# Performance work log

Measured on AMD Instinct MI355X. Metric: run time of the kernel, lower is better.

## Reference

```python
import jax, jax.numpy as jnp
import numpy as np

B, S, DIM = 2, 2048, 1024
H, DH = 16, 64
WIN = 512


def setup_inputs() -> dict:
    key = jax.random.key(0)
    k1, k2, k3 = jax.random.split(key, 3)
    x = jax.random.normal(k1, (B, S, DIM), dtype=jnp.float32)
    Wqkv = jax.random.normal(k2, (DIM, 3 * H * DH), dtype=jnp.float32) * (DIM ** -0.5)
    Wout = jax.random.normal(k3, (H * DH, DIM), dtype=jnp.float32) * ((H * DH) ** -0.5)
    return {"x": x, "Wqkv": Wqkv, "Wout": Wout}


def reference(x, Wqkv, Wout):
    b, s, _ = x.shape
    qkv = jnp.einsum('bsd,de->bse', x, Wqkv)  # (B,S,3*H*DH)
    q, k, v = jnp.split(qkv, 3, axis=-1)
    # -> (B,H,S,DH)
    q = q.reshape(b, s, H, DH).transpose(0, 2, 1, 3)
    k = k.reshape(b, s, H, DH).transpose(0, 2, 1, 3)
    v = v.reshape(b, s, H, DH).transpose(0, 2, 1, 3)
    scale = DH ** -0.5  # attention sees per-head dim
    scores = jnp.einsum('bhsd,bhtd->bhst', q, k) * scale  # dense (B,H,S,S)
    i = jnp.arange(s)[:, None]
    j = jnp.arange(s)[None, :]
    mask = (j >= i - WIN + 1) & (j <= i)  # causal sliding window
    mask_value = -jnp.finfo(scores.dtype).max
    scores = jnp.where(mask[None, None], scores, mask_value)
    attn = jax.nn.softmax(scores, axis=-1)
    out = jnp.einsum('bhst,bhtd->bhsd', attn, v)
    out = out.transpose(0, 2, 1, 3).reshape(b, s, H * DH)
    return jnp.einsum('bse,ed->bsd', out, Wout)
```

## Files before the change

kernel.cpp:

```cpp
#include <hip/hip_runtime.h>

#define S_LEN 2048
#define BATCH 2
#define HDIM 1024
#define NH 16
#define DH 64
#define WINSZ 512
#define MROWS (BATCH * S_LEN)

typedef __attribute__((ext_vector_type(8))) short bfrag;
typedef __attribute__((ext_vector_type(4))) float f32x4;
typedef __attribute__((ext_vector_type(4))) int i128;

__device__ __forceinline__ short f2bf(float f) {
    union { float f; unsigned u; } v;
    v.f = f;
    unsigned r = v.u + 0x7fffu + ((v.u >> 16) & 1u);
    return (short)(r >> 16);
}

__device__ __forceinline__ void gload_lds16(const short* g, short* l) {
    __builtin_amdgcn_global_load_lds(
        (const __attribute__((address_space(1))) unsigned int*)g,
        (__attribute__((address_space(3))) unsigned int*)l, 16, 0, 0);
}

__global__ __launch_bounds__(256)
void prep_kernel(const float* __restrict__ x, const float* __restrict__ Wqkv,
                 const float* __restrict__ Wout,
                 short* __restrict__ x_bf, short* __restrict__ wqkv_t, short* __restrict__ wout_t)
{
    __shared__ float tile[32][33];
    const int bid = blockIdx.x;
    const int t = threadIdx.x;

    if (bid < 4096) {
        int i = bid * 256 + t;
        float4 v = ((const float4*)x)[i];
        union { short s[4]; int2 p; } u;
        u.s[0] = f2bf(v.x); u.s[1] = f2bf(v.y); u.s[2] = f2bf(v.z); u.s[3] = f2bf(v.w);
        ((int2*)x_bf)[i] = u.p;
        return;
    }

    const float* in;
    short* out;
    int R, C, bx, by;
    if (bid < 7168) {
        int lb = bid - 4096;
        in = Wqkv; out = wqkv_t; R = 1024; C = 3072;
        bx = lb % 96; by = lb / 96;
    } else {
        int lb = bid - 7168;
        in = Wout; out = wout_t; R = 1024; C = 1024;
        bx = lb & 31; by = lb >> 5;
    }
    int tc0 = bx * 32, tr0 = by * 32;
    int c = t & 31, r0 = t >> 5;
    #pragma unroll
    for (int k = 0; k < 4; ++k) {
        int r = r0 + k * 8;
        tile[r][c] = in[(size_t)(tr0 + r) * C + tc0 + c];
    }
    __syncthreads();
    int r2p = (t & 15) << 1, c0 = t >> 4;
    #pragma unroll
    for (int k = 0; k < 2; ++k) {
        int c2 = c0 + k * 16;
        union { short sh[2]; int w; } u;
        u.sh[0] = f2bf(tile[r2p][c2]);
        u.sh[1] = f2bf(tile[r2p + 1][c2]);
        *(int*)(&out[(size_t)(tc0 + c2) * R + tr0 + r2p]) = u.w;
    }
}

__global__ __launch_bounds__(256, 3)
void gemm_qkv(const short* __restrict__ A, const short* __restrict__ Bt,
              short* __restrict__ qk_rm, short* __restrict__ vto)
{
    __shared__ __align__(16) short smraw[17408];
    short (*Al)[4096] = (short(*)[4096])smraw;
    short (*Bl)[4096] = (short(*)[4096])(smraw + 8192);
    const int K = HDIM;
    const int t = threadIdx.x;
    const int lane = t & 63;
    const int wave = t >> 6;
    const int wr = wave >> 1, wc = wave & 1;
    const int m0 = blockIdx.y * 128, n0 = blockIdx.x * 128;
    const int lq = lane & 15;
    const int g = lane >> 4;
    const int lk8 = g << 3;

    f32x4 acc[4][4];
    #pragma unroll
    for (int m = 0; m < 4; ++m)
        #pragma unroll
        for (int n = 0; n < 4; ++n)
            acc[m][n] = (f32x4){0.f, 0.f, 0.f, 0.f};

    const int row0s = t >> 2, col0s = (t & 3) << 3;
    const int row1s = (256 + t) >> 2;
    const size_t dst0 = (size_t)(wave * 64) * 8;
    const size_t dst1 = (size_t)(256 + wave * 64) * 8;

    auto stage = [&](int k0, int sb) {
        gload_lds16(&A[(size_t)(m0 + row0s) * K + k0 + col0s], &Al[sb][0] + dst0);
        gload_lds16(&Bt[(size_t)(n0 + row0s) * K + k0 + col0s], &Bl[sb][0] + dst0);
        gload_lds16(&A[(size_t)(m0 + row1s) * K + k0 + col0s], &Al[sb][0] + dst1);
        gload_lds16(&Bt[(size_t)(n0 + row1s) * K + k0 + col0s], &Bl[sb][0] + dst1);
    };

    const int nk = K >> 5;
    stage(0, 0);
    __syncthreads();
    for (int ki = 0; ki < nk; ++ki) {
        const int cur = ki & 1;
        if (ki + 1 < nk) stage((ki + 1) << 5, cur ^ 1);
        bfrag af[4], bfr[4];
        #pragma unroll
        for (int m = 0; m < 4; ++m)
            af[m] = *(const bfrag*)(&Al[cur][(wr * 64 + m * 16 + lq) * 32 + lk8]);
        #pragma unroll
        for (int n = 0; n < 4; ++n)
            bfr[n] = *(const bfrag*)(&Bl[cur][(wc * 64 + n * 16 + lq) * 32 + lk8]);
        #pragma unroll
        for (int m = 0; m < 4; ++m)
            #pragma unroll
            for (int n = 0; n < 4; ++n)
                acc[m][n] = __builtin_amdgcn_mfma_f32_16x16x32_bf16(af[m], bfr[n], acc[m][n], 0, 0, 0);
        __syncthreads();
    }

    if (n0 < 2048) {
        #pragma unroll
        for (int m = 0; m < 4; ++m)
            #pragma unroll
            for (int n = 0; n < 4; ++n) {
                int col = n0 + wc * 64 + n * 16 + lq;
                int row0 = m0 + wr * 64 + m * 16 + g * 4;
                #pragma unroll
                for (int r = 0; r < 4; ++r)
                    qk_rm[(size_t)(row0 + r) * 2048 + col] = f2bf(acc[m][n][r]);
            }
    } else {
        short* T = smraw;
        #pragma unroll
        for (int m = 0; m < 4; ++m)
            #pragma unroll
            for (int n = 0; n < 4; ++n) {
                int cl = wc * 64 + n * 16 + lq;
                int rl0 = wr * 64 + m * 16 + g * 4;
                union { short sh[4]; int2 w; } u;
                #pragma unroll
                for (int r = 0; r < 4; ++r) u.sh[r] = f2bf(acc[m][n][r]);
                *(int2*)(&T[cl * 136 + rl0]) = u.w;
            }
        __syncthreads();
        const int b = m0 >> 11, sbase = m0 & 2047;
        const int h0 = (n0 - 2048) >> 6;
        #pragma unroll
        for (int i = 0; i < 8; ++i) {
            int c2 = i * 256 + t;
            int rv = c2 >> 4;
            int sc = (c2 & 15) << 3;
            int h = h0 + (rv >> 6), dh = rv & 63;
            i128 v = *(const i128*)(&T[rv * 136 + sc]);
            *(i128*)(&vto[((size_t)((b * NH + h) * DH + dh)) * S_LEN + sbase + sc]) = v;
        }
    }
}

__global__ __launch_bounds__(256, 2)
void gemm_out(const short* __restrict__ A, const short* __restrict__ Bt,
              float* __restrict__ co)
{
    __shared__ __align__(16) short Al[2][128 * 64];
    __shared__ __align__(16) short Bl[2][128 * 64];
    const int K = HDIM, N = HDIM;
    const int t = threadIdx.x;
    const int lane = t & 63;
    const int wave = t >> 6;
    const int wr = wave >> 1, wc = wave & 1;
    const int m0 = blockIdx.y * 128, n0 = blockIdx.x * 128;
    const int lq = lane & 15;
    const int g = lane >> 4;

    f32x4 acc[4][4];
    #pragma unroll
    for (int m = 0; m < 4; ++m)
        #pragma unroll
        for (int n = 0; n < 4; ++n)
            acc[m][n] = (f32x4){0.f, 0.f, 0.f, 0.f};

    auto stage = [&](int k0, int sb) {
        #pragma unroll
        for (int q = 0; q < 4; ++q) {
            int chunk = q * 256 + t;
            int row = chunk >> 3, col = (chunk & 7) << 3;
            size_t dst = (size_t)(q * 256 + wave * 64) * 8;
            gload_lds16(&A[(size_t)(m0 + row) * K + k0 + col], &Al[sb][0] + dst);
            gload_lds16(&Bt[(size_t)(n0 + row) * K + k0 + col], &Bl[sb][0] + dst);
        }
    };

    const int nk = K >> 6;
    stage(0, 0);
    for (int ki = 0; ki < nk; ++ki) {
        const int cur = ki & 1;
        if (ki + 1 < nk) {
            stage((ki + 1) << 6, cur ^ 1);
            asm volatile("s_waitcnt vmcnt(8)" ::: "memory");
        } else {
            asm volatile("s_waitcnt vmcnt(0)" ::: "memory");
        }
        __builtin_amdgcn_sched_barrier(0);
        __builtin_amdgcn_s_barrier();
        __builtin_amdgcn_sched_barrier(0);
        bfrag af[4][2], bfr[4][2];
        #pragma unroll
        for (int m = 0; m < 4; ++m)
            #pragma unroll
            for (int ks = 0; ks < 2; ++ks)
                af[m][ks] = *(const bfrag*)(&Al[cur][(wr * 64 + m * 16 + lq) * 64 + ks * 32 + (g << 3)]);
        #pragma unroll
        for (int n = 0; n < 4; ++n)
            #pragma unroll
            for (int ks = 0; ks < 2; ++ks)
                bfr[n][ks] = *(const bfrag*)(&Bl[cur][(wc * 64 + n * 16 + lq) * 64 + ks * 32 + (g << 3)]);
        #pragma unroll
        for (int m = 0; m < 4; ++m)
            #pragma unroll
            for (int n = 0; n < 4; ++n) {
                acc[m][n] = __builtin_amdgcn_mfma_f32_16x16x32_bf16(af[m][0], bfr[n][0], acc[m][n], 0, 0, 0);
                acc[m][n] = __builtin_amdgcn_mfma_f32_16x16x32_bf16(af[m][1], bfr[n][1], acc[m][n], 0, 0, 0);
            }
        asm volatile("s_waitcnt lgkmcnt(0)" ::: "memory");
        __builtin_amdgcn_sched_barrier(0);
        __builtin_amdgcn_s_barrier();
        __builtin_amdgcn_sched_barrier(0);
    }

    #pragma unroll
    for (int m = 0; m < 4; ++m)
        #pragma unroll
        for (int n = 0; n < 4; ++n) {
            int col = n0 + wc * 64 + n * 16 + lq;
            int row0 = m0 + wr * 64 + m * 16 + g * 4;
            #pragma unroll
            for (int r = 0; r < 4; ++r)
                co[(size_t)(row0 + r) * N + col] = acc[m][n][r];
        }
}

__global__ __launch_bounds__(256, 4)
void attn_kernel(const short* __restrict__ qk, const short* __restrict__ vt,
                 short* __restrict__ attno)
{
    __shared__ __align__(16) short Kl[2][64 * 64];
    __shared__ __align__(16) short Vl[2][64 * 64];
    __shared__ __align__(16) short Pl[4][16 * 64];

    const int bid = blockIdx.x;
    const int logical = (bid & 7) * 128 + (bid >> 3);
    const int qblk = logical & 31;
    const int bh = logical >> 5;
    const int b = bh >> 4, h = bh & 15;

    const int t = threadIdx.x;
    const int wave = t >> 6, lane = t & 63;
    const int qb0 = qblk * 64;
    const int i0 = qb0 + wave * 16;
    const short* qbase = qk + (size_t)b * S_LEN * 2048 + h * 64;
    const short* kbase = qk + (size_t)b * S_LEN * 2048 + 1024 + h * 64;
    const short* vp = vt + (size_t)bh * DH * S_LEN;
    char* myP = (char*)&Pl[wave][0];

    const int lq = lane & 15;
    const int g = lane >> 4;
    const int swz = (lq & 7) << 4;
    const int l7 = lq & 7;
    const int qi = i0 + lq;

    bfrag qf[2];
    qf[0] = *(const bfrag*)(&qbase[(size_t)(i0 + lq) * 2048 + (g << 3)]);
    qf[1] = *(const bfrag*)(&qbase[(size_t)(i0 + lq) * 2048 + 32 + (g << 3)]);

    f32x4 oacc[4];
    #pragma unroll
    for (int d = 0; d < 4; ++d) oacc[d] = (f32x4){0.f, 0.f, 0.f, 0.f};
    float m2 = -1e30f, lrun = 0.f, scale_prev = 1.f;
    const float QSCALE = 0.125f * 1.44269504f;

    bfrag pf_prev[2];
    bfrag vf_prev[2][4];

    int j_lo = qb0 - (WINSZ - 1);
    if (j_lo < 0) j_lo = 0;
    j_lo &= ~63;
    const int nT = ((qb0 + 64) - j_lo) >> 6;

    auto stage = [&](int jrel, short* kbuf, short* vbuf) {
        #pragma unroll
        for (int qq = 0; qq < 2; ++qq) {
            int chunk = qq * 256 + wave * 64 + lane;
            int row = chunk >> 3;
            int cc = (chunk & 7) ^ (row & 7);
            short* kdst = kbuf + (size_t)(qq * 256 + wave * 64) * 8;
            short* vdst = vbuf + (size_t)(qq * 256 + wave * 64) * 8;
            gload_lds16(kbase + (size_t)(j_lo + jrel + row) * 2048 + cc * 8, kdst);
            gload_lds16(vp + (size_t)row * S_LEN + j_lo + jrel + cc * 8, vdst);
        }
    };

    stage(0, Kl[0], Vl[0]);

    for (int ti = 0; ti < nT; ++ti) {
        const int cur = ti & 1;
        const int j0 = j_lo + ti * 64;
        const bool more = (ti + 1 < nT);
        if (more) stage((ti + 1) * 64, Kl[cur ^ 1], Vl[cur ^ 1]);

        if (ti > 0) {
            #pragma unroll
            for (int d = 0; d < 4; ++d) {
                f32x4 o = oacc[d];
                o[0] *= scale_prev; o[1] *= scale_prev; o[2] *= scale_prev; o[3] *= scale_prev;
                oacc[d] = o;
            }
            __builtin_amdgcn_s_setprio(1);
            #pragma unroll
            for (int kt = 0; kt < 2; ++kt)
                #pragma unroll
                for (int d = 0; d < 4; ++d)
                    oacc[d] = __builtin_amdgcn_mfma_f32_16x16x32_bf16(vf_prev[kt][d], pf_prev[kt], oacc[d], 0, 0, 0);
            __builtin_amdgcn_s_setprio(0);
        }

        if (more) asm volatile("s_waitcnt vmcnt(4)" ::: "memory");
        else      asm volatile("s_waitcnt vmcnt(0)" ::: "memory");
        __builtin_amdgcn_sched_barrier(0);
        __builtin_amdgcn_s_barrier();
        __builtin_amdgcn_sched_barrier(0);

        const short* Kc = Kl[cur];
        const short* Vc = Vl[cur];

        f32x4 sc[4];
        __builtin_amdgcn_s_setprio(1);
        #pragma unroll
        for (int tc = 0; tc < 4; ++tc) {
            bfrag a0 = *(const bfrag*)(&Kc[(tc * 16 + lq) * 64 + ((g ^ l7) << 3)]);
            bfrag a1 = *(const bfrag*)(&Kc[(tc * 16 + lq) * 64 + (((4 | g) ^ l7) << 3)]);
            f32x4 z = (f32x4){0.f, 0.f, 0.f, 0.f};
            z = __builtin_amdgcn_mfma_f32_16x16x32_bf16(a0, qf[0], z, 0, 0, 0);
            z = __builtin_amdgcn_mfma_f32_16x16x32_bf16(a1, qf[1], z, 0, 0, 0);
            sc[tc] = z;
        }
        __builtin_amdgcn_s_setprio(0);

        const bool nomask = (j0 >= i0 - (WINSZ - 16)) && (j0 + 63 <= i0);
        float s[4][4];
        float pm = -1e30f;
        #pragma unroll
        for (int tc = 0; tc < 4; ++tc)
            #pragma unroll
            for (int r = 0; r < 4; ++r) {
                float sv = sc[tc][r] * QSCALE;
                if (!nomask) {
                    int kj = j0 + tc * 16 + 4 * g + r;
                    sv = ((kj <= qi) && (kj > qi - WINSZ)) ? sv : -1e30f;
                }
                s[tc][r] = sv;
                pm = fmaxf(pm, sv);
            }
        pm = fmaxf(pm, __shfl_xor(pm, 16));
        pm = fmaxf(pm, __shfl_xor(pm, 32));
        float mnew = fmaxf(m2, pm);
        float scale_i = exp2f(m2 - mnew);
        m2 = mnew;
        float p[4][4];
        float rs = 0.f;
        #pragma unroll
        for (int tc = 0; tc < 4; ++tc)
            #pragma unroll
            for (int r = 0; r < 4; ++r) {
                p[tc][r] = exp2f(s[tc][r] - mnew);
                rs += p[tc][r];
            }
        rs += __shfl_xor(rs, 16);
        rs += __shfl_xor(rs, 32);
        lrun = lrun * scale_i + rs;
        scale_prev = scale_i;

        #pragma unroll
        for (int tc = 0; tc < 4; ++tc) {
            union { short sh[4]; int2 w; } u;
            u.sh[0] = f2bf(p[tc][0]); u.sh[1] = f2bf(p[tc][1]);
            u.sh[2] = f2bf(p[tc][2]); u.sh[3] = f2bf(p[tc][3]);
            int wb = (lq * 128 + tc * 32 + g * 8) ^ swz;
            *(int2*)(myP + wb) = u.w;
        }
        #pragma unroll
        for (int kt = 0; kt < 2; ++kt) {
            int rb = (lq * 128 + kt * 64 + g * 16) ^ swz;
            pf_prev[kt] = *(const bfrag*)(myP + rb);
            #pragma unroll
            for (int d = 0; d < 4; ++d)
                vf_prev[kt][d] = *(const bfrag*)(&Vc[(d * 16 + lq) * 64 + (((kt * 4 + g) ^ l7) << 3)]);
        }
        asm volatile("s_waitcnt lgkmcnt(0)" ::: "memory");
        __builtin_amdgcn_sched_barrier(0);
        __builtin_amdgcn_s_barrier();
        __builtin_amdgcn_sched_barrier(0);
    }

    #pragma unroll
    for (int d = 0; d < 4; ++d) {
        f32x4 o = oacc[d];
        o[0] *= scale_prev; o[1] *= scale_prev; o[2] *= scale_prev; o[3] *= scale_prev;
        oacc[d] = o;
    }
    #pragma unroll
    for (int kt = 0; kt < 2; ++kt)
        #pragma unroll
        for (int d = 0; d < 4; ++d)
            oacc[d] = __builtin_amdgcn_mfma_f32_16x16x32_bf16(vf_prev[kt][d], pf_prev[kt], oacc[d], 0, 0, 0);

    const float inv_l = 1.f / lrun;
    size_t rowbase = ((size_t)(b * S_LEN + qi)) * HDIM + h * DH;
    #pragma unroll
    for (int d = 0; d < 4; ++d) {
        union { short sh[4]; int2 w; } u;
        #pragma unroll
        for (int r = 0; r < 4; ++r)
            u.sh[r] = f2bf(oacc[d][r] * inv_l);
        *(int2*)(&attno[rowbase + d * 16 + 4 * g]) = u.w;
    }
}

extern "C" void kernel_launch(void* const* d_in, const int* in_sizes, int n_in,
                              void* d_out, int out_size, void* d_ws, size_t ws_size,
                              hipStream_t stream) {
    const float* x = (const float*)d_in[0];
    const float* Wqkv = (const float*)d_in[1];
    const float* Wout = (const float*)d_in[2];
    float* out = (float*)d_out;
    char* ws = (char*)d_ws;

    short* x_bf   = (short*)(ws);
    short* wqkv_t = (short*)(ws + 8388608);
    short* wout_t = (short*)(ws + 14680064);
    short* qk_rm  = (short*)(ws + 16777216);
    short* v_t    = (short*)(ws + 33554432);
    short* attno  = x_bf;

    prep_kernel<<<8192, 256, 0, stream>>>(x, Wqkv, Wout, x_bf, wqkv_t, wout_t);
    gemm_qkv<<<dim3(24, 32), 256, 0, stream>>>(x_bf, wqkv_t, qk_rm, v_t);
    attn_kernel<<<dim3(BATCH * NH * (S_LEN / 64)), 256, 0, stream>>>(qk_rm, v_t, attno);
    gemm_out<<<dim3(8, 32), 256, 0, stream>>>(attno, wout_t, out);
}
```

Baseline: 164.6 us.

## Use explicit waitcnt barriers in GEMM loop and lazy softmax rescaling

In the GEMM main loop, __syncthreads is replaced by explicit vmcnt/lgkmcnt waits plus raw s_barrier. This lets the prefetch for the next K tile stay in flight while the current tile is consumed. In the attention kernel, the running-max update and the rescale of the output accumulator are skipped whenever the new tile max stays within a threshold (8 in log2 units) of the current max across the wave. This removes the exp and vector multiplies in the common case, in exchange for a wave-wide vote and a small risk of larger exponent values in bf16/fp32.

```diff
diff --git a/kernel.cpp b/kernel.cpp
--- a/kernel.cpp
+++ b/kernel.cpp
@@ -112,10 +112,17 @@
 
     const int nk = K >> 5;
     stage(0, 0);
-    __syncthreads();
     for (int ki = 0; ki < nk; ++ki) {
         const int cur = ki & 1;
-        if (ki + 1 < nk) stage((ki + 1) << 5, cur ^ 1);
+        if (ki + 1 < nk) {
+            stage((ki + 1) << 5, cur ^ 1);
+            asm volatile("s_waitcnt vmcnt(4)" ::: "memory");
+        } else {
+            asm volatile("s_waitcnt vmcnt(0)" ::: "memory");
+        }
+        __builtin_amdgcn_sched_barrier(0);
+        __builtin_amdgcn_s_barrier();
+        __builtin_amdgcn_sched_barrier(0);
         bfrag af[4], bfr[4];
         #pragma unroll
         for (int m = 0; m < 4; ++m)
@@ -128,7 +135,10 @@
             #pragma unroll
             for (int n = 0; n < 4; ++n)
                 acc[m][n] = __builtin_amdgcn_mfma_f32_16x16x32_bf16(af[m], bfr[n], acc[m][n], 0, 0, 0);
-        __syncthreads();
+        asm volatile("s_waitcnt lgkmcnt(0)" ::: "memory");
+        __builtin_amdgcn_sched_barrier(0);
+        __builtin_amdgcn_s_barrier();
+        __builtin_amdgcn_sched_barrier(0);
     }
 
     if (n0 < 2048) {
@@ -289,6 +299,7 @@
     #pragma unroll
     for (int d = 0; d < 4; ++d) oacc[d] = (f32x4){0.f, 0.f, 0.f, 0.f};
     float m2 = -1e30f, lrun = 0.f, scale_prev = 1.f;
+    bool defer_prev = true;
     const float QSCALE = 0.125f * 1.44269504f;
 
     bfrag pf_prev[2];
@@ -321,11 +332,13 @@
         if (more) stage((ti + 1) * 64, Kl[cur ^ 1], Vl[cur ^ 1]);
 
         if (ti > 0) {
-            #pragma unroll
-            for (int d = 0; d < 4; ++d) {
-                f32x4 o = oacc[d];
-                o[0] *= scale_prev; o[1] *= scale_prev; o[2] *= scale_prev; o[3] *= scale_prev;
-                oacc[d] = o;
+            if (!defer_prev) {
+                #pragma unroll
+                for (int d = 0; d < 4; ++d) {
+                    f32x4 o = oacc[d];
+                    o[0] *= scale_prev; o[1] *= scale_prev; o[2] *= scale_prev; o[3] *= scale_prev;
+                    oacc[d] = o;
+                }
             }
             __builtin_amdgcn_s_setprio(1);
             #pragma unroll
@@ -375,22 +388,27 @@
             }
         pm = fmaxf(pm, __shfl_xor(pm, 16));
         pm = fmaxf(pm, __shfl_xor(pm, 32));
-        float mnew = fmaxf(m2, pm);
-        float scale_i = exp2f(m2 - mnew);
-        m2 = mnew;
+        bool defer_i = __all(pm <= m2 + 8.f);
+        float scale_i = 1.f;
+        if (!defer_i) {
+            float mnew = fmaxf(m2, pm);
+            scale_i = exp2f(m2 - mnew);
+            m2 = mnew;
+        }
         float p[4][4];
         float rs = 0.f;
         #pragma unroll
         for (int tc = 0; tc < 4; ++tc)
             #pragma unroll
             for (int r = 0; r < 4; ++r) {
-                p[tc][r] = exp2f(s[tc][r] - mnew);
+                p[tc][r] = exp2f(s[tc][r] - m2);
                 rs += p[tc][r];
             }
         rs += __shfl_xor(rs, 16);
         rs += __shfl_xor(rs, 32);
         lrun = lrun * scale_i + rs;
         scale_prev = scale_i;
+        defer_prev = defer_i;
 
         #pragma unroll
         for (int tc = 0; tc < 4; ++tc) {
@@ -414,11 +432,13 @@
         __builtin_amdgcn_sched_barrier(0);
     }
 
-    #pragma unroll
-    for (int d = 0; d < 4; ++d) {
-        f32x4 o = oacc[d];
-        o[0] *= scale_prev; o[1] *= scale_prev; o[2] *= scale_prev; o[3] *= scale_prev;
-        oacc[d] = o;
+    if (!defer_prev) {
+        #pragma unroll
+        for (int d = 0; d < 4; ++d) {
+            f32x4 o = oacc[d];
+            o[0] *= scale_prev; o[1] *= scale_prev; o[2] *= scale_prev; o[3] *= scale_prev;
+            oacc[d] = o;
+        }
     }
     #pragma unroll
     for (int kt = 0; kt < 2; ++kt)
```

New measurement: 165.1 us. About the same (+0.3%).
